# Optimization experiments

Hardware: AMD Instinct MI355X
Metric: run time of the kernel (lower is better)

Reference implementation:

```python
import jax, jax.numpy as jnp
import numpy as np

S = 4          # num_segments
T = 4096       # frames
D = 1024       # input_size == output_size
HEADS = 1
FREQ = 10000.0
DH = D // HEADS     # per-head width = 1024
TB = T // S         # block height = 1024
WB = DH // S        # block width  = 256


def _abs_pos(tb, d, freq):
    # Matches getAbsolutePosition: AP[p, 2i] = sin(p / freq^(2i/d)), AP[p, 2i+1] = cos(same).
    pos = jnp.arange(tb, dtype=jnp.float32)[:, None]          # [tb,1]
    i = jnp.arange(tb // 2, dtype=jnp.float32)[None, :]       # [1,tb//2]
    ang = pos / jnp.power(jnp.float32(freq), 2.0 * i / d)     # [tb,tb//2]
    ap = jnp.zeros((tb, tb), jnp.float32)
    return ap.at[:, 0::2].set(jnp.sin(ang)).at[:, 1::2].set(jnp.cos(ang))


def setup_inputs() -> dict:
    key = jax.random.key(0)
    ks = jax.random.split(key, 6)
    x = jax.random.normal(ks[0], (T, D), jnp.float32)
    Wq = jax.random.normal(ks[1], (HEADS, DH, D), jnp.float32) * 0.02
    Wk = jax.random.normal(ks[2], (HEADS, DH, D), jnp.float32) * 0.02
    Wv = jax.random.normal(ks[3], (HEADS, DH, D), jnp.float32) * 0.02
    Wout = jax.random.normal(ks[4], (D, D), jnp.float32) * 0.02
    Wout2 = jax.random.normal(ks[5], (WB, WB + 2), jnp.float32) * 0.05
    return {"x": x, "Wq": Wq, "Wk": Wk, "Wv": Wv, "Wout": Wout, "Wout2": Wout2}


def _forward(x, Wq, Wk, Wv, Wout, Wout2):
    # diversity = 1 - cosine similarity (F.normalize p=2 along dim=1)
    xu = x / jnp.maximum(jnp.linalg.norm(x, axis=1, keepdims=True), 1e-12)
    div = 1.0 - xu @ xu.T                                     # [T,T]

    Q = jnp.einsum('ti,hdi->htd', x, Wq)                      # [h,T,DH]
    K = jnp.einsum('ti,hdi->htd', x, Wk)
    V = jnp.einsum('ti,hdi->htd', x, Wv)

    def blk(A):  # [h,T,DH] -> [h,S*S,TB,WB], block (i,j) row-major as in local_x/local_y
        return A.reshape(-1, S, TB, S, WB).transpose(0, 1, 3, 2, 4).reshape(-1, S * S, TB, WB)

    qb, kb, vb = blk(Q), blk(K), blk(V)
    # diversity uses the diagonal row-block for every column-block j of row i
    drow = jnp.stack([div[i * TB:(i + 1) * TB, i * TB:(i + 1) * TB] for i in range(S)], 0)  # [S,TB,TB]
    db = jnp.repeat(drow, S, axis=0)[None]                    # [1,S*S,TB,TB]

    sim = jnp.einsum('hbqc,hbkc->hbqk', qb, kb) + _abs_pos(TB, D, FREQ)  # [h,S*S,TB,TB]
    attw = jax.nn.softmax(sim, axis=-1)
    # normalized row entropy, then L1-normalized (F.normalize p=1)
    ent = -(attw * jax.nn.log_softmax(sim, axis=-1)).sum(-1) / jnp.log(jnp.float32(TB))  # [h,S*S,TB]
    ent = ent / jnp.maximum(jnp.abs(ent).sum(-1, keepdims=True), 1e-12)

    dep = (db * attw).sum(-1) / db.sum(-1)                    # [h,S*S,TB]
    att_win = attw + dep[:, :, None, :] * attw                # dep_factor rows are identical
    ctx = jnp.einsum('hbqk,hbkc->hbqc', att_win, vb)          # [h,S*S,TB,WB]

    chars = jax.lax.stop_gradient(jnp.stack([ent, dep], axis=-1))  # [h,S*S,TB,2] (detach)
    y = jnp.concatenate([ctx, chars], axis=-1) @ Wout2.T      # [h,S*S,TB,WB]

    # reassemble grid of blocks back to [h,T,DH], concat heads, final projection
    y = y.reshape(-1, S, S, TB, WB).transpose(0, 1, 3, 2, 4).reshape(-1, T, DH)
    y = y.transpose(1, 0, 2).reshape(T, HEADS * DH)
    return y @ Wout.T                                         # [T,D]


def reference(x, Wq, Wk, Wv, Wout, Wout2):
    return _forward(x, Wq, Wk, Wv, Wout, Wout2)
```

## Files before the change

### kernel.cpp

```cpp
#include <hip/hip_runtime.h>
#include <hip/hip_bf16.h>

#define TT 4096
#define DD 1024
#define TBB 1024
#define WBB 256

typedef __attribute__((ext_vector_type(8))) _Float16 half8;
typedef __attribute__((ext_vector_type(4))) _Float16 half4;
typedef __attribute__((ext_vector_type(16))) float f32x16;

__device__ __forceinline__ unsigned short f2h(float v) {
  _Float16 h = (_Float16)v;
  return *reinterpret_cast<unsigned short*>(&h);
}
__device__ __forceinline__ float h2f(unsigned short u) {
  _Float16 h = *reinterpret_cast<_Float16*>(&u);
  return (float)h;
}

__device__ __forceinline__ void gl_lds16(const unsigned short* g, unsigned short* l) {
  __builtin_amdgcn_global_load_lds(
      (const __attribute__((address_space(1))) void*)(unsigned long long)(g),
      (__attribute__((address_space(3))) void*)(unsigned long long)(l),
      16, 0, 0);
}

__device__ __forceinline__ float waveSum(float v) {
#pragma unroll
  for (int o = 32; o > 0; o >>= 1) v += __shfl_down(v, o, 64);
  return v;
}
__device__ __forceinline__ float bSum(float v) {
#pragma unroll
  for (int o = 32; o > 0; o >>= 1) v += __shfl_xor(v, o, 64);
  return v;
}
__device__ __forceinline__ float bMax(float v) {
#pragma unroll
  for (int o = 32; o > 0; o >>= 1) v = fmaxf(v, __shfl_xor(v, o, 64));
  return v;
}

template <int EPI, typename OutT>
__global__ __launch_bounds__(256) void gemm_bt(
    const unsigned short* __restrict__ A, const unsigned short* __restrict__ B,
    OutT* __restrict__ C,
    int K, int lda, int ldb, int ldc,
    int zbase, int zdiv,
    long sAi, long sAj, long sBi, long sBj, long sCi, long sCj,
    long sAz, long sBz, long sCz,
    const float* __restrict__ e0, const float* __restrict__ e1,
    const float* __restrict__ e2, const float* __restrict__ e3)
{
  __shared__ __align__(16) unsigned short lA[2][4096];
  __shared__ __align__(16) unsigned short lB[2][4096];

  const int z = blockIdx.z, gz = zbase + z;
  const int zi = gz / zdiv, zj = gz - zi * zdiv;
  const unsigned short* Ab = A + (long)zi * sAi + (long)zj * sAj + (long)z * sAz;
  const unsigned short* Bb = B + (long)zi * sBi + (long)zj * sBj + (long)z * sBz;
  const long offC = (long)zi * sCi + (long)zj * sCj + (long)z * sCz;

  const int m0 = blockIdx.y * 128, n0 = blockIdx.x * 128;
  const int tid = threadIdx.x, wave = tid >> 6, lane = tid & 63;
  const int wm = (wave >> 1) * 64, wn = (wave & 1) * 64;
  const int srow = lane >> 2;
  const int scol = (((lane & 3) ^ ((srow >> 1) & 3))) * 8;
  const int l31 = lane & 31, khi = lane >> 5;
  const int sw2 = (l31 >> 1) & 3;

  f32x16 acc[2][2] = {};

  for (int k0 = 0; k0 < K; k0 += 64) {
#pragma unroll
    for (int h = 0; h < 2; ++h)
#pragma unroll
      for (int t = 0; t < 2; ++t) {
        const int r = wave * 32 + t * 16 + srow;
        gl_lds16(Ab + (long)(m0 + r) * lda + (k0 + h * 32 + scol), &lA[h][wave * 1024 + t * 512]);
        gl_lds16(Bb + (long)(n0 + r) * ldb + (k0 + h * 32 + scol), &lB[h][wave * 1024 + t * 512]);
      }
    __syncthreads();

    half8 af[2][4], bfr[2][4];
#pragma unroll
    for (int mi = 0; mi < 2; ++mi)
#pragma unroll
      for (int ks = 0; ks < 4; ++ks)
        af[mi][ks] = *(const half8*)&lA[ks >> 1][(wm + mi * 32 + l31) * 32 + ((((ks & 1) * 2 + khi) ^ sw2) * 8)];
#pragma unroll
    for (int ni = 0; ni < 2; ++ni)
#pragma unroll
      for (int ks = 0; ks < 4; ++ks)
        bfr[ni][ks] = *(const half8*)&lB[ks >> 1][(wn + ni * 32 + l31) * 32 + ((((ks & 1) * 2 + khi) ^ sw2) * 8)];

#pragma unroll
    for (int ks = 0; ks < 4; ++ks)
#pragma unroll
      for (int mi = 0; mi < 2; ++mi)
#pragma unroll
        for (int ni = 0; ni < 2; ++ni)
          acc[mi][ni] = __builtin_amdgcn_mfma_f32_32x32x16_f16(af[mi][ks], bfr[ni][ks], acc[mi][ni], 0, 0, 0);
    __syncthreads();
  }

  OutT* Cb = C + offC;
#pragma unroll
  for (int mi = 0; mi < 2; ++mi)
#pragma unroll
    for (int ni = 0; ni < 2; ++ni)
#pragma unroll
      for (int r = 0; r < 16; ++r) {
        const int row = m0 + wm + mi * 32 + khi * 4 + (r & 3) + 8 * (r >> 2);
        const int col = n0 + wn + ni * 32 + l31;
        float v = acc[mi][ni][r];
        const long ci = (long)row * ldc + col;
        if constexpr (sizeof(OutT) == 2) {
          Cb[ci] = (OutT)f2h(v);
        } else {
          Cb[ci] = v;
        }
      }
}

template <int EPI, typename OutT>
__global__ __launch_bounds__(256) void gemm_s(
    const unsigned short* __restrict__ A, const unsigned short* __restrict__ B,
    OutT* __restrict__ C,
    int K, int lda, int ldb, int ldc,
    int zbase, int zdiv,
    long sAi, long sAj, long sBi, long sBj, long sCi, long sCj,
    long sAz, long sBz, long sCz,
    const float* __restrict__ e0, const float* __restrict__ e1,
    const float* __restrict__ e2, const float* __restrict__ e3)
{
  __shared__ __align__(16) unsigned short lA[2][2048];
  __shared__ __align__(16) unsigned short lB[2][2048];

  if constexpr (EPI == 2) {
    if (blockIdx.x < blockIdx.y) return;
  }

  const int z = blockIdx.z, gz = zbase + z;
  const int zi = gz / zdiv, zj = gz - zi * zdiv;
  const unsigned short* Ab = A + (long)zi * sAi + (long)zj * sAj + (long)z * sAz;
  const unsigned short* Bb = B + (long)zi * sBi + (long)zj * sBj + (long)z * sBz;
  const long offC = (long)zi * sCi + (long)zj * sCj + (long)z * sCz;

  const int m0 = blockIdx.y * 64, n0 = blockIdx.x * 64;
  const int tid = threadIdx.x, wave = tid >> 6, lane = tid & 63;
  const int wm = (wave >> 1) * 32, wn = (wave & 1) * 32;
  const int srow = lane >> 2;
  const int grow = wave * 16 + srow;
  const int scol = (((lane & 3) ^ ((grow >> 1) & 3))) * 8;
  const int l31 = lane & 31, khi = lane >> 5;
  const int sw2 = (l31 >> 1) & 3;

  f32x16 acc = {};

  for (int k0 = 0; k0 < K; k0 += 64) {
#pragma unroll
    for (int h = 0; h < 2; ++h) {
      gl_lds16(Ab + (long)(m0 + grow) * lda + (k0 + h * 32 + scol), &lA[h][wave * 512]);
      gl_lds16(Bb + (long)(n0 + grow) * ldb + (k0 + h * 32 + scol), &lB[h][wave * 512]);
    }
    __syncthreads();

    half8 af[4], bfr[4];
#pragma unroll
    for (int ks = 0; ks < 4; ++ks) {
      af[ks] = *(const half8*)&lA[ks >> 1][(wm + l31) * 32 + ((((ks & 1) * 2 + khi) ^ sw2) * 8)];
      bfr[ks] = *(const half8*)&lB[ks >> 1][(wn + l31) * 32 + ((((ks & 1) * 2 + khi) ^ sw2) * 8)];
    }
#pragma unroll
    for (int ks = 0; ks < 4; ++ks)
      acc = __builtin_amdgcn_mfma_f32_32x32x16_f16(af[ks], bfr[ks], acc, 0, 0, 0);
    __syncthreads();
  }

  OutT* Cb = C + offC;
#pragma unroll
  for (int r = 0; r < 16; ++r) {
    const int row = m0 + wm + khi * 4 + (r & 3) + 8 * (r >> 2);
    const int col = n0 + wn + l31;
    float v = acc[r];
    if constexpr (EPI == 1 || EPI == 2) v = 1.0f - v;
    if constexpr (EPI == 3)
      v += e0[(long)gz * 1024 + row] * e2[col] + e1[(long)gz * 1024 + row] * e3[col];
    const long ci = (long)row * ldc + col;
    if constexpr (sizeof(OutT) == 2) {
      Cb[ci] = (OutT)f2h(v);
    } else {
      Cb[ci] = v;
    }
  }

  if constexpr (EPI == 2) {
    if (blockIdx.x != blockIdx.y) {
      unsigned short* mir = &lA[0][0];
      const int lc = wn + l31;
#pragma unroll
      for (int chunk = 0; chunk < 2; ++chunk) {
        __syncthreads();
        if ((lc >> 5) == chunk) {
#pragma unroll
          for (int r = 0; r < 16; ++r) {
            const int lr = wm + khi * 4 + (r & 3) + 8 * (r >> 2);
            mir[(lc & 31) * 68 + lr] = f2h(1.0f - acc[r]);
          }
        }
        __syncthreads();
        const int cl = tid >> 3, co = (tid & 7) * 8;
        const ushort4 a = *(const ushort4*)&mir[cl * 68 + co];
        const ushort4 b = *(const ushort4*)&mir[cl * 68 + co + 4];
        unsigned short* dst = (unsigned short*)Cb + (long)(n0 + chunk * 32 + cl) * ldc + m0 + co;
        *(ushort4*)dst = a;
        *(ushort4*)(dst + 4) = b;
      }
    }
  }
}

__global__ __launch_bounds__(256) void sim_gemm(
    const unsigned short* __restrict__ A, const unsigned short* __restrict__ B,
    unsigned short* __restrict__ C,
    const unsigned short* __restrict__ APh)
{
  __shared__ __align__(16) unsigned short lA[2][4096];
  __shared__ __align__(16) unsigned short lB[2][4096];

  const int gz = blockIdx.z;
  const int zi = gz >> 2, zj = gz & 3;
  const unsigned short* Ab = A + (long)zi * (TBB * DD) + zj * WBB;
  const unsigned short* Bb = B + (long)zi * (TBB * DD) + zj * WBB;
  unsigned short* Cb = C + (long)gz * TBB * TBB;

  const int m0 = blockIdx.y * 128, n0 = blockIdx.x * 128;
  const int tid = threadIdx.x, wave = tid >> 6, lane = tid & 63;
  const int wm = (wave >> 1) * 64, wn = (wave & 1) * 64;
  const int srow = lane >> 2;
  const int scol = ((lane & 3) ^ ((srow >> 1) & 3)) * 8;
  const int l31 = lane & 31, khi = lane >> 5;
  const int sw2 = (l31 >> 1) & 3;

  f32x16 acc[2][2] = {};

  for (int k0 = 0; k0 < WBB; k0 += 64) {
#pragma unroll
    for (int h = 0; h < 2; ++h)
#pragma unroll
      for (int t = 0; t < 2; ++t) {
        const int r = wave * 32 + t * 16 + srow;
        gl_lds16(Ab + (long)(m0 + r) * DD + (k0 + h * 32 + scol), &lA[h][wave * 1024 + t * 512]);
        gl_lds16(Bb + (long)(n0 + r) * DD + (k0 + h * 32 + scol), &lB[h][wave * 1024 + t * 512]);
      }
    __syncthreads();

    half8 af[2][4], bfr[2][4];
#pragma unroll
    for (int mi = 0; mi < 2; ++mi)
#pragma unroll
      for (int ks = 0; ks < 4; ++ks)
        af[mi][ks] = *(const half8*)&lA[ks >> 1][(wm + mi * 32 + l31) * 32 + ((((ks & 1) * 2 + khi) ^ sw2) * 8)];
#pragma unroll
    for (int ni = 0; ni < 2; ++ni)
#pragma unroll
      for (int ks = 0; ks < 4; ++ks)
        bfr[ni][ks] = *(const half8*)&lB[ks >> 1][(wn + ni * 32 + l31) * 32 + ((((ks & 1) * 2 + khi) ^ sw2) * 8)];

#pragma unroll
    for (int ks = 0; ks < 4; ++ks)
#pragma unroll
      for (int mi = 0; mi < 2; ++mi)
#pragma unroll
        for (int ni = 0; ni < 2; ++ni)
          acc[mi][ni] = __builtin_amdgcn_mfma_f32_32x32x16_f16(af[mi][ks], bfr[ni][ks], acc[mi][ni], 0, 0, 0);
    __syncthreads();
  }

#pragma unroll
  for (int mi = 0; mi < 2; ++mi)
#pragma unroll
    for (int ni = 0; ni < 2; ++ni)
#pragma unroll
      for (int r = 0; r < 16; ++r) {
        const int row = m0 + wm + mi * 32 + khi * 4 + (r & 3) + 8 * (r >> 2);
        const int col = n0 + wn + ni * 32 + l31;
        Cb[(long)row * TBB + col] = f2h(acc[mi][ni][r] + h2f(APh[(long)row * 1024 + col]));
      }
}

__global__ __launch_bounds__(256) void ctx_gemm_s(
    const unsigned short* __restrict__ simh, const float* __restrict__ dep,
    const float* __restrict__ Brow,
    const unsigned short* __restrict__ Vt, unsigned short* __restrict__ ctx)
{
  __shared__ __align__(16) unsigned short lA[2][2048];
  __shared__ __align__(16) unsigned short lB[2][2048];
  __shared__ __align__(16) unsigned short sDepH[1024];

  const int gz = blockIdx.z, zi = gz >> 2, zj = gz & 3;
  const int m0 = blockIdx.y * 64, n0 = blockIdx.x * 64;
  const int tid = threadIdx.x, wave = tid >> 6, lane = tid & 63;
  const int wm = (wave >> 1) * 32, wn = (wave & 1) * 32;
  const int srow = lane >> 2;
  const int grow = wave * 16 + srow;
  const int scol = ((lane & 3) ^ ((grow >> 1) & 3)) * 8;
  const int l31 = lane & 31, khi = lane >> 5;
  const int sw2 = (l31 >> 1) & 3;

#pragma unroll
  for (int p = 0; p < 4; ++p)
    sDepH[tid + p * 256] = f2h(1.f + dep[(long)gz * 1024 + tid + p * 256]);
  __syncthreads();

  const float B0 = Brow[(long)gz * 1024 + m0 + (tid >> 3)];
  const float B1 = Brow[(long)gz * 1024 + m0 + 32 + (tid >> 3)];

  const unsigned short* Ab = simh + (long)gz * TBB * TBB;
  const unsigned short* Bb = Vt + (long)(zj * 256) * TT + (long)zi * 1024;

  f32x16 acc = {};

  for (int k0 = 0; k0 < 1024; k0 += 64) {
#pragma unroll
    for (int h = 0; h < 2; ++h)
      gl_lds16(Bb + (long)(n0 + grow) * TT + (k0 + h * 32 + scol), &lB[h][wave * 512]);
#pragma unroll
    for (int h = 0; h < 2; ++h)
#pragma unroll
      for (int p = 0; p < 2; ++p) {
        const int idx = p * 1024 + tid * 4;
        const int row = idx >> 5, col = idx & 31;
        const ushort4 wv = *(const ushort4*)(Ab + (long)(m0 + row) * 1024 + k0 + h * 32 + col);
        const float Bp = p ? B1 : B0;
        half4 ev;
        ev.x = (_Float16)exp2f(fmaf(h2f(wv.x), 1.4426950408889634f, -Bp));
        ev.y = (_Float16)exp2f(fmaf(h2f(wv.y), 1.4426950408889634f, -Bp));
        ev.z = (_Float16)exp2f(fmaf(h2f(wv.z), 1.4426950408889634f, -Bp));
        ev.w = (_Float16)exp2f(fmaf(h2f(wv.w), 1.4426950408889634f, -Bp));
        const half4 dv = *(const half4*)&sDepH[k0 + h * 32 + col];
        half4 pv = ev * dv;
        const int pcol = (((col >> 3) ^ ((row >> 1) & 3)) << 3) | (col & 7);
        *(half4*)&lA[h][row * 32 + pcol] = pv;
      }
    __syncthreads();

    half8 af[4], bfr[4];
#pragma unroll
    for (int ks = 0; ks < 4; ++ks) {
      af[ks] = *(const half8*)&lA[ks >> 1][(wm + l31) * 32 + ((((ks & 1) * 2 + khi) ^ sw2) * 8)];
      bfr[ks] = *(const half8*)&lB[ks >> 1][(wn + l31) * 32 + ((((ks & 1) * 2 + khi) ^ sw2) * 8)];
    }
#pragma unroll
    for (int ks = 0; ks < 4; ++ks)
      acc = __builtin_amdgcn_mfma_f32_32x32x16_f16(af[ks], bfr[ks], acc, 0, 0, 0);
    __syncthreads();
  }

  unsigned short* Cb = ctx + (long)gz * TBB * WBB;
#pragma unroll
  for (int r = 0; r < 16; ++r) {
    const int row = m0 + wm + khi * 4 + (r & 3) + 8 * (r >> 2);
    const int col = n0 + wn + l31;
    Cb[(long)row * WBB + col] = f2h(acc[r]);
  }
}

__global__ __launch_bounds__(256) void prepx_kernel(
    const float* __restrict__ x, unsigned short* __restrict__ xh,
    unsigned short* __restrict__ xu)
{
  const int t = blockIdx.x, tid = threadIdx.x;
  const float4 v = *((const float4*)(x + (long)t * DD) + tid);
  float ss = v.x * v.x + v.y * v.y + v.z * v.z + v.w * v.w;
  ss = waveSum(ss);
  __shared__ float red[4];
  if ((tid & 63) == 0) red[tid >> 6] = ss;
  __syncthreads();
  const float tot = red[0] + red[1] + red[2] + red[3];
  const float inv = 1.f / fmaxf(sqrtf(tot), 1e-12f);
  ushort4 h, u;
  h.x = f2h(v.x); h.y = f2h(v.y); h.z = f2h(v.z); h.w = f2h(v.w);
  u.x = f2h(v.x * inv); u.y = f2h(v.y * inv); u.z = f2h(v.z * inv); u.w = f2h(v.w * inv);
  *((ushort4*)(xh + (long)t * DD) + tid) = h;
  *((ushort4*)(xu + (long)t * DD) + tid) = u;
}

__global__ __launch_bounds__(256) void castall_kernel(
    const float* __restrict__ Wq, const float* __restrict__ Wk,
    const float* __restrict__ Wv, const float* __restrict__ Wo,
    unsigned short* __restrict__ Wh, unsigned short* __restrict__ WoB)
{
  const long idx4 = ((long)blockIdx.x * 256 + threadIdx.x) * 4;
  const int which = (int)(idx4 >> 20);
  const long loc = idx4 & ((1L << 20) - 1);
  const float* src = (which == 0) ? Wq : ((which == 1) ? Wk : ((which == 2) ? Wv : Wo));
  unsigned short* dst = (which < 3) ? (Wh + idx4) : (WoB + loc);
  const float4 v = *(const float4*)(src + loc);
  ushort4 h;
  h.x = f2h(v.x); h.y = f2h(v.y); h.z = f2h(v.z); h.w = f2h(v.w);
  *(ushort4*)dst = h;
}

__global__ __launch_bounds__(256) void packw2_kernel(
    const float* __restrict__ W2, unsigned short* __restrict__ W2B,
    float* __restrict__ Ecol, float* __restrict__ Dcol)
{
  const int c = blockIdx.x, j = threadIdx.x;
  W2B[c * 256 + j] = f2h(W2[c * 258 + j]);
  if (j == 0) {
    Ecol[c] = W2[c * 258 + 256];
    Dcol[c] = W2[c * 258 + 257];
  }
}

__global__ __launch_bounds__(256) void ap_kernel(unsigned short* __restrict__ APh)
{
  const int p = blockIdx.x, tid = threadIdx.x;
#pragma unroll
  for (int t = 0; t < 4; ++t) {
    const int col = tid + t * 256;
    const int i = col >> 1;
    const float e = (2.0f * (float)i) / 1024.0f;
    const float ang = (float)p * exp2f(e * -13.287712379549449f);
    APh[(long)p * 1024 + col] = f2h((col & 1) ? cosf(ang) : sinf(ang));
  }
}

__global__ __launch_bounds__(256) void stats_kernel(
    const unsigned short* __restrict__ sim, const unsigned short* __restrict__ divb,
    float* __restrict__ dep, float* __restrict__ ent,
    float* __restrict__ Brow)
{
  const int gz = blockIdx.y, bi = gz >> 2;
  const int wave = threadIdx.x >> 6, lane = threadIdx.x & 63;
  const int q = blockIdx.x * 4 + wave;
  const unsigned short* srow = sim + ((long)gz * TBB + q) * TBB;
  const unsigned short* drow = divb + ((long)bi * TBB + q) * TBB;
  float s[16], d[16];
#pragma unroll
  for (int u = 0; u < 4; ++u) {
    const ushort4 sv = *(const ushort4*)(srow + u * 256 + lane * 4);
    const ushort4 dv = *(const ushort4*)(drow + u * 256 + lane * 4);
    s[u * 4 + 0] = h2f(sv.x); s[u * 4 + 1] = h2f(sv.y);
    s[u * 4 + 2] = h2f(sv.z); s[u * 4 + 3] = h2f(sv.w);
    d[u * 4 + 0] = h2f(dv.x); d[u * 4 + 1] = h2f(dv.y);
    d[u * 4 + 2] = h2f(dv.z); d[u * 4 + 3] = h2f(dv.w);
  }
  float m = s[0];
#pragma unroll
  for (int i = 1; i < 16; ++i) m = fmaxf(m, s[i]);
  m = bMax(m);
  const float mB = m * 1.4426950408889634f;
  float l = 0.f, ss = 0.f, dn = 0.f, ds = 0.f;
#pragma unroll
  for (int i = 0; i < 16; ++i) {
    const float e = exp2f(fmaf(s[i], 1.4426950408889634f, -mB));
    l += e; ss += e * s[i]; dn += e * d[i]; ds += d[i];
  }
  l = bSum(l); ss = bSum(ss); dn = bSum(dn); ds = bSum(ds);
  if (lane == 0) {
    const long o = (long)gz * TBB + q;
    const float Li = 1.f / l;
    const float lnL = logf(l);
    dep[o] = (dn * Li) / ds;
    ent[o] = (m + lnL - ss * Li) * 0.14426950408889634f;
    Brow[o] = (m + lnL) * 1.4426950408889634f;
  }
}

__global__ __launch_bounds__(256) void entnorm_kernel(float* __restrict__ ent)
{
  const int gz = blockIdx.x, tid = threadIdx.x;
  float s = 0.f;
#pragma unroll
  for (int p = 0; p < 4; ++p) s += fabsf(ent[(long)gz * TBB + tid + p * 256]);
  s = waveSum(s);
  __shared__ float red[4];
  if ((tid & 63) == 0) red[tid >> 6] = s;
  __syncthreads();
  const float scale = 1.f / fmaxf(red[0] + red[1] + red[2] + red[3], 1e-12f);
#pragma unroll
  for (int p = 0; p < 4; ++p) ent[(long)gz * TBB + tid + p * 256] *= scale;
}

extern "C" void kernel_launch(void* const* d_in, const int* in_sizes, int n_in,
                              void* d_out, int out_size, void* d_ws, size_t ws_size,
                              hipStream_t stream)
{
  const float* x  = (const float*)d_in[0];
  const float* Wq = (const float*)d_in[1];
  const float* Wk = (const float*)d_in[2];
  const float* Wv = (const float*)d_in[3];
  const float* Wo = (const float*)d_in[4];
  const float* W2 = (const float*)d_in[5];

  char* ws = (char*)d_ws;
  size_t off = 0;
  auto take = [&](size_t bytes) -> void* {
    void* p = ws + off;
    off += (bytes + 255) & ~(size_t)255;
    return p;
  };
  unsigned short* QKV = (unsigned short*)take((size_t)2 * TT * DD * 2);
  unsigned short* xh  = (unsigned short*)take((size_t)TT * DD * 2);
  unsigned short* xu  = (unsigned short*)take((size_t)TT * DD * 2);
  unsigned short* Wh  = (unsigned short*)take((size_t)3 * DD * DD * 2);
  unsigned short* WoB = (unsigned short*)take((size_t)DD * DD * 2);
  unsigned short* W2B = (unsigned short*)take((size_t)256 * 256 * 2);
  float* Ecol = (float*)take(256 * 4);
  float* Dcol = (float*)take(256 * 4);
  unsigned short* APh = (unsigned short*)take((size_t)TBB * TBB * 2);
  unsigned short* divb = (unsigned short*)take((size_t)4 * TBB * TBB * 2);
  unsigned short* Vt = (unsigned short*)take((size_t)DD * TT * 2);
  unsigned short* simh = (unsigned short*)take((size_t)16 * TBB * TBB * 2);
  float* depb = (float*)take((size_t)16 * TBB * 4);
  float* entb = (float*)take((size_t)16 * TBB * 4);
  float* Brow = (float*)take((size_t)16 * TBB * 4);
  unsigned short* ctx = (unsigned short*)take((size_t)16 * TBB * WBB * 2);
  unsigned short* Y = (unsigned short*)take((size_t)TT * DD * 2);
  (void)ws_size; (void)in_sizes; (void)n_in; (void)out_size;

  prepx_kernel<<<TT, 256, 0, stream>>>(x, xh, xu);
  castall_kernel<<<(4 * DD * DD) / 1024, 256, 0, stream>>>(Wq, Wk, Wv, Wo, Wh, WoB);
  packw2_kernel<<<256, 256, 0, stream>>>(W2, W2B, Ecol, Dcol);
  ap_kernel<<<TBB, 256, 0, stream>>>(APh);

  gemm_bt<0, unsigned short><<<dim3(DD / 128, TT / 128, 2), 256, 0, stream>>>(
      xh, Wh, QKV,
      DD, DD, DD, DD, 0, 1,
      0, 0, (long)DD * DD, 0, (long)TT * DD, 0,
      0, 0, 0, nullptr, nullptr, nullptr, nullptr);

  gemm_s<0, unsigned short><<<dim3(TT / 64, DD / 64, 1), 256, 0, stream>>>(
      Wh + (size_t)2 * DD * DD, xh, Vt,
      DD, DD, DD, TT, 0, 1,
      0, 0, 0, 0, 0, 0,
      0, 0, 0, nullptr, nullptr, nullptr, nullptr);

  gemm_s<2, unsigned short><<<dim3(16, 16, 4), 256, 0, stream>>>(
      xu, xu, divb,
      DD, DD, DD, TBB, 0, 1,
      (long)TBB * DD, 0, (long)TBB * DD, 0, (long)TBB * TBB, 0,
      0, 0, 0, nullptr, nullptr, nullptr, nullptr);

  const unsigned short* Qh = QKV;
  const unsigned short* Kh = QKV + (size_t)TT * DD;

  sim_gemm<<<dim3(8, 8, 16), 256, 0, stream>>>(Qh, Kh, simh, APh);

  stats_kernel<<<dim3(TBB / 4, 16), 256, 0, stream>>>(simh, divb, depb, entb, Brow);
  entnorm_kernel<<<16, 256, 0, stream>>>(entb);

  ctx_gemm_s<<<dim3(4, 16, 16), 256, 0, stream>>>(simh, depb, Brow, Vt, ctx);

  gemm_s<3, unsigned short><<<dim3(4, 16, 16), 256, 0, stream>>>(
      ctx, W2B, Y,
      WBB, WBB, WBB, DD, 0, 4,
      (long)4 * TBB * WBB, (long)TBB * WBB, 0, 0, (long)TBB * DD, (long)WBB,
      0, 0, 0, entb, depb, Ecol, Dcol);

  gemm_s<0, float><<<dim3(16, 64, 1), 256, 0, stream>>>(
      Y, WoB, (float*)d_out,
      DD, DD, DD, DD, 0, 1,
      0, 0, 0, 0, 0, 0,
      0, 0, 0, nullptr, nullptr, nullptr, nullptr);
}
```

Baseline: 251.9 us.

## Fold Wout2 into Wout and fuse char-feature epilogue into final projection

Precomputes a combined weight WF = Wout·blockdiag(Wout2) and folded entropy/dependency column vectors, so the per-block Wout2 GEMM and its intermediate Y buffer disappear. Context is written directly in the reassembled [T,D] layout, and the entropy/dep terms are added in the final GEMM epilogue via the folded vectors. Entropy normalization is merged with the fold computation into one small kernel, and the AP table uses sincos per pair. It adds a small weight-fold GEMM per call and changes rounding order in fp16.

```diff
diff --git a/kernel.cpp b/kernel.cpp
--- a/kernel.cpp
+++ b/kernel.cpp
@@ -180,14 +180,27 @@
   }
 
   OutT* Cb = C + offC;
+  float Ef[4], Df[4];
+  if constexpr (EPI == 4) {
+    const int col0 = n0 + wn + l31;
+#pragma unroll
+    for (int j = 0; j < 4; ++j) {
+      Ef[j] = e2[j * 1024 + col0];
+      Df[j] = e3[j * 1024 + col0];
+    }
+  }
 #pragma unroll
   for (int r = 0; r < 16; ++r) {
     const int row = m0 + wm + khi * 4 + (r & 3) + 8 * (r >> 2);
     const int col = n0 + wn + l31;
     float v = acc[r];
     if constexpr (EPI == 1 || EPI == 2) v = 1.0f - v;
-    if constexpr (EPI == 3)
-      v += e0[(long)gz * 1024 + row] * e2[col] + e1[(long)gz * 1024 + row] * e3[col];
+    if constexpr (EPI == 4) {
+      const float4 en = *(const float4*)(e0 + (long)row * 4);
+      const float4 dp = *(const float4*)(e1 + (long)row * 4);
+      v += en.x * Ef[0] + en.y * Ef[1] + en.z * Ef[2] + en.w * Ef[3]
+         + dp.x * Df[0] + dp.y * Df[1] + dp.z * Df[2] + dp.w * Df[3];
+    }
     const long ci = (long)row * ldc + col;
     if constexpr (sizeof(OutT) == 2) {
       Cb[ci] = (OutT)f2h(v);
@@ -292,9 +305,9 @@
 }
 
 __global__ __launch_bounds__(256) void ctx_gemm_s(
-    const unsigned short* __restrict__ simh, const float* __restrict__ dep,
+    const unsigned short* __restrict__ simh, const float* __restrict__ dep2,
     const float* __restrict__ Brow,
-    const unsigned short* __restrict__ Vt, unsigned short* __restrict__ ctx)
+    const unsigned short* __restrict__ Vt, unsigned short* __restrict__ ctxR)
 {
   __shared__ __align__(16) unsigned short lA[2][2048];
   __shared__ __align__(16) unsigned short lB[2][2048];
@@ -312,7 +325,8 @@
 
 #pragma unroll
   for (int p = 0; p < 4; ++p)
-    sDepH[tid + p * 256] = f2h(1.f + dep[(long)gz * 1024 + tid + p * 256]);
+    sDepH[tid + p * 256] =
+        f2h(1.f + dep2[((long)zi * 1024 + tid + p * 256) * 4 + zj]);
   __syncthreads();
 
   const float B0 = Brow[(long)gz * 1024 + m0 + (tid >> 3)];
@@ -359,12 +373,11 @@
     __syncthreads();
   }
 
-  unsigned short* Cb = ctx + (long)gz * TBB * WBB;
 #pragma unroll
   for (int r = 0; r < 16; ++r) {
     const int row = m0 + wm + khi * 4 + (r & 3) + 8 * (r >> 2);
     const int col = n0 + wn + l31;
-    Cb[(long)row * WBB + col] = f2h(acc[r]);
+    ctxR[((long)zi * 1024 + row) * 1024 + zj * 256 + col] = f2h(acc[r]);
   }
 }
 
@@ -405,14 +418,14 @@
 }
 
 __global__ __launch_bounds__(256) void packw2_kernel(
-    const float* __restrict__ W2, unsigned short* __restrict__ W2B,
+    const float* __restrict__ W2, unsigned short* __restrict__ W2T,
     float* __restrict__ Ecol, float* __restrict__ Dcol)
 {
-  const int c = blockIdx.x, j = threadIdx.x;
-  W2B[c * 256 + j] = f2h(W2[c * 258 + j]);
-  if (j == 0) {
-    Ecol[c] = W2[c * 258 + 256];
-    Dcol[c] = W2[c * 258 + 257];
+  const int w = blockIdx.x, c = threadIdx.x;
+  W2T[c * 256 + w] = f2h(W2[w * 258 + c]);
+  if (c == 0) {
+    Ecol[w] = W2[w * 258 + 256];
+    Dcol[w] = W2[w * 258 + 257];
   }
 }
 
@@ -420,18 +433,21 @@
 {
   const int p = blockIdx.x, tid = threadIdx.x;
 #pragma unroll
-  for (int t = 0; t < 4; ++t) {
-    const int col = tid + t * 256;
-    const int i = col >> 1;
-    const float e = (2.0f * (float)i) / 1024.0f;
+  for (int t = 0; t < 2; ++t) {
+    const int pr = tid + t * 256;
+    const float e = (float)pr * (1.0f / 512.0f);
     const float ang = (float)p * exp2f(e * -13.287712379549449f);
-    APh[(long)p * 1024 + col] = f2h((col & 1) ? cosf(ang) : sinf(ang));
+    float s, c;
+    sincosf(ang, &s, &c);
+    ushort2 o;
+    o.x = f2h(s); o.y = f2h(c);
+    *(ushort2*)(APh + (long)p * 1024 + 2 * pr) = o;
   }
 }
 
 __global__ __launch_bounds__(256) void stats_kernel(
     const unsigned short* __restrict__ sim, const unsigned short* __restrict__ divb,
-    float* __restrict__ dep, float* __restrict__ ent,
+    float* __restrict__ dep2, float* __restrict__ ent2,
     float* __restrict__ Brow)
 {
   const int gz = blockIdx.y, bi = gz >> 2;
@@ -462,28 +478,62 @@
   }
   l = bSum(l); ss = bSum(ss); dn = bSum(dn); ds = bSum(ds);
   if (lane == 0) {
-    const long o = (long)gz * TBB + q;
     const float Li = 1.f / l;
     const float lnL = logf(l);
-    dep[o] = (dn * Li) / ds;
-    ent[o] = (m + lnL - ss * Li) * 0.14426950408889634f;
-    Brow[o] = (m + lnL) * 1.4426950408889634f;
-  }
-}
-
-__global__ __launch_bounds__(256) void entnorm_kernel(float* __restrict__ ent)
-{
-  const int gz = blockIdx.x, tid = threadIdx.x;
-  float s = 0.f;
-#pragma unroll
-  for (int p = 0; p < 4; ++p) s += fabsf(ent[(long)gz * TBB + tid + p * 256]);
-  s = waveSum(s);
-  __shared__ float red[4];
-  if ((tid & 63) == 0) red[tid >> 6] = s;
-  __syncthreads();
-  const float scale = 1.f / fmaxf(red[0] + red[1] + red[2] + red[3], 1e-12f);
-#pragma unroll
-  for (int p = 0; p < 4; ++p) ent[(long)gz * TBB + tid + p * 256] *= scale;
+    const long o2 = ((long)bi * 1024 + q) * 4 + (gz & 3);
+    dep2[o2] = (dn * Li) / ds;
+    ent2[o2] = (m + lnL - ss * Li) * 0.14426950408889634f;
+    Brow[(long)gz * TBB + q] = (m + lnL) * 1.4426950408889634f;
+  }
+}
+
+__global__ __launch_bounds__(256) void prefinal_kernel(
+    float* __restrict__ ent2, const float* __restrict__ Ecol,
+    const float* __restrict__ Dcol, const float* __restrict__ Wo,
+    float* __restrict__ Efold, float* __restrict__ Dfold)
+{
+  const int b = blockIdx.x, tid = threadIdx.x;
+  if (b < 4) {
+    float4 v[4];
+    float4 a = {0.f, 0.f, 0.f, 0.f};
+#pragma unroll
+    for (int p = 0; p < 4; ++p) {
+      v[p] = *(const float4*)(ent2 + ((long)b * 1024 + tid + p * 256) * 4);
+      a.x += fabsf(v[p].x); a.y += fabsf(v[p].y);
+      a.z += fabsf(v[p].z); a.w += fabsf(v[p].w);
+    }
+    a.x = waveSum(a.x); a.y = waveSum(a.y);
+    a.z = waveSum(a.z); a.w = waveSum(a.w);
+    __shared__ float red[4][4];
+    if ((tid & 63) == 0) {
+      const int w = tid >> 6;
+      red[w][0] = a.x; red[w][1] = a.y; red[w][2] = a.z; red[w][3] = a.w;
+    }
+    __syncthreads();
+    float4 sc;
+    sc.x = 1.f / fmaxf(red[0][0] + red[1][0] + red[2][0] + red[3][0], 1e-12f);
+    sc.y = 1.f / fmaxf(red[0][1] + red[1][1] + red[2][1] + red[3][1], 1e-12f);
+    sc.z = 1.f / fmaxf(red[0][2] + red[1][2] + red[2][2] + red[3][2], 1e-12f);
+    sc.w = 1.f / fmaxf(red[0][3] + red[1][3] + red[2][3] + red[3][3], 1e-12f);
+#pragma unroll
+    for (int p = 0; p < 4; ++p) {
+      float4 o = v[p];
+      o.x *= sc.x; o.y *= sc.y; o.z *= sc.z; o.w *= sc.w;
+      *(float4*)(ent2 + ((long)b * 1024 + tid + p * 256) * 4) = o;
+    }
+  } else {
+    const int idx = (b - 4) * 256 + tid;
+    const int j = idx >> 10, d = idx & 1023;
+    const float* wrow = Wo + (long)d * 1024 + j * 256;
+    float se = 0.f, sd = 0.f;
+    for (int w = 0; w < 256; ++w) {
+      const float wv = wrow[w];
+      se += Ecol[w] * wv;
+      sd += Dcol[w] * wv;
+    }
+    Efold[j * 1024 + d] = se;
+    Dfold[j * 1024 + d] = sd;
+  }
 }
 
 extern "C" void kernel_launch(void* const* d_in, const int* in_sizes, int n_in,
@@ -509,24 +559,32 @@
   unsigned short* xu  = (unsigned short*)take((size_t)TT * DD * 2);
   unsigned short* Wh  = (unsigned short*)take((size_t)3 * DD * DD * 2);
   unsigned short* WoB = (unsigned short*)take((size_t)DD * DD * 2);
-  unsigned short* W2B = (unsigned short*)take((size_t)256 * 256 * 2);
+  unsigned short* W2T = (unsigned short*)take((size_t)256 * 256 * 2);
+  unsigned short* WFh = (unsigned short*)take((size_t)DD * DD * 2);
   float* Ecol = (float*)take(256 * 4);
   float* Dcol = (float*)take(256 * 4);
+  float* Efold = (float*)take((size_t)4 * DD * 4);
+  float* Dfold = (float*)take((size_t)4 * DD * 4);
   unsigned short* APh = (unsigned short*)take((size_t)TBB * TBB * 2);
   unsigned short* divb = (unsigned short*)take((size_t)4 * TBB * TBB * 2);
   unsigned short* Vt = (unsigned short*)take((size_t)DD * TT * 2);
   unsigned short* simh = (unsigned short*)take((size_t)16 * TBB * TBB * 2);
-  float* depb = (float*)take((size_t)16 * TBB * 4);
-  float* entb = (float*)take((size_t)16 * TBB * 4);
+  float* dep2 = (float*)take((size_t)TT * 4 * 4);
+  float* ent2 = (float*)take((size_t)TT * 4 * 4);
   float* Brow = (float*)take((size_t)16 * TBB * 4);
-  unsigned short* ctx = (unsigned short*)take((size_t)16 * TBB * WBB * 2);
-  unsigned short* Y = (unsigned short*)take((size_t)TT * DD * 2);
+  unsigned short* ctxR = (unsigned short*)take((size_t)TT * DD * 2);
   (void)ws_size; (void)in_sizes; (void)n_in; (void)out_size;
 
   prepx_kernel<<<TT, 256, 0, stream>>>(x, xh, xu);
   castall_kernel<<<(4 * DD * DD) / 1024, 256, 0, stream>>>(Wq, Wk, Wv, Wo, Wh, WoB);
-  packw2_kernel<<<256, 256, 0, stream>>>(W2, W2B, Ecol, Dcol);
+  packw2_kernel<<<256, 256, 0, stream>>>(W2, W2T, Ecol, Dcol);
   ap_kernel<<<TBB, 256, 0, stream>>>(APh);
+
+  gemm_s<0, unsigned short><<<dim3(4, 16, 4), 256, 0, stream>>>(
+      WoB, W2T, WFh,
+      256, DD, 256, DD, 0, 4,
+      0, 256, 0, 0, 0, 256,
+      0, 0, 0, nullptr, nullptr, nullptr, nullptr);
 
   gemm_bt<0, unsigned short><<<dim3(DD / 128, TT / 128, 2), 256, 0, stream>>>(
       xh, Wh, QKV,
@@ -551,20 +609,15 @@
 
   sim_gemm<<<dim3(8, 8, 16), 256, 0, stream>>>(Qh, Kh, simh, APh);
 
-  stats_kernel<<<dim3(TBB / 4, 16), 256, 0, stream>>>(simh, divb, depb, entb, Brow);
-  entnorm_kernel<<<16, 256, 0, stream>>>(entb);
-
-  ctx_gemm_s<<<dim3(4, 16, 16), 256, 0, stream>>>(simh, depb, Brow, Vt, ctx);
-
-  gemm_s<3, unsigned short><<<dim3(4, 16, 16), 256, 0, stream>>>(
-      ctx, W2B, Y,
-      WBB, WBB, WBB, DD, 0, 4,
-      (long)4 * TBB * WBB, (long)TBB * WBB, 0, 0, (long)TBB * DD, (long)WBB,
-      0, 0, 0, entb, depb, Ecol, Dcol);
-
-  gemm_s<0, float><<<dim3(16, 64, 1), 256, 0, stream>>>(
-      Y, WoB, (float*)d_out,
+  stats_kernel<<<dim3(TBB / 4, 16), 256, 0, stream>>>(simh, divb, dep2, ent2, Brow);
+
+  prefinal_kernel<<<20, 256, 0, stream>>>(ent2, Ecol, Dcol, Wo, Efold, Dfold);
+
+  ctx_gemm_s<<<dim3(4, 16, 16), 256, 0, stream>>>(simh, dep2, Brow, Vt, ctxR);
+
+  gemm_s<4, float><<<dim3(16, 64, 1), 256, 0, stream>>>(
+      ctxR, WFh, (float*)d_out,
       DD, DD, DD, DD, 0, 1,
       0, 0, 0, 0, 0, 0,
-      0, 0, 0, nullptr, nullptr, nullptr, nullptr);
-}
+      0, 0, 0, ent2, dep2, Efold, Dfold);
+}
```

New measurement: 255.4 us. About the same (+1.4%).
